# Optimization experiments

Measured on AMD Instinct MI355X. Metric: run time of the kernel, lower is better.

The kernel has to match this reference:

```python
import jax, jax.numpy as jnp
import numpy as np

# Constants from the torch module
S_DECAY = 0.95    # sentence_decay
P_DECAY = 0.99    # paragraph_decay
D_DECAY = 0.999   # document_decay
ALPHA = 0.1       # delta_update alpha for sentence/paragraph
DOC_ALPHA = 0.05  # delta_update alpha for document
BETA = 1.0
PARA_GROUP = 5    # sentences per paragraph
EPS = 1e-12       # F.normalize eps


def _normalize(x):
    # matches torch.nn.functional.normalize(x, dim=-1)
    return x / jnp.maximum(jnp.linalg.norm(x, axis=-1, keepdims=True), EPS)


def _delta_step(M, kn, v, alpha, beta):
    # M: [H, dk, dv]; kn: [dk] (already L2-normalized); v: [dv]
    # M_new = M @ (I - alpha * kn kn^T) + beta * kn v^T   (erase matrix is symmetric,
    # so the einsum 'hkv,hkj->hjv' form equals this rank-1 update -- no dk x dk matrix needed)
    kTM = jnp.einsum('k,hkv->hv', kn, M)                       # [H, dv]
    return M - alpha * kn[None, :, None] * kTM[:, None, :] \
             + beta * (kn[:, None] * v[None, :])[None, :, :]


def _scan_updates(M0, K, V, decay, alpha, beta):
    # Streaming delta-rule: per step, decay then erase/write.
    def step(M, kv):
        k, v = kv
        M = M * decay
        M = _delta_step(M, _normalize(k), v, alpha, beta)
        return M, None
    M, _ = jax.lax.scan(step, M0, (K, V))
    return M


def setup_inputs() -> dict:
    key = jax.random.key(0)
    ks = jax.random.split(key, 7)
    T, d_emb, d_k, d_v, H = 1000, 768, 256, 256, 8
    emb = jax.random.normal(ks[0], (T, d_emb), dtype=jnp.float32)
    q = jax.random.normal(ks[1], (d_k,), dtype=jnp.float32)
    W_k = jax.random.normal(ks[2], (d_emb, d_k), dtype=jnp.float32) * 0.02
    b_k = jax.random.normal(ks[3], (d_k,), dtype=jnp.float32) * 0.02
    W_v = jax.random.normal(ks[4], (d_emb, d_v), dtype=jnp.float32) * 0.02
    b_v = jax.random.normal(ks[5], (d_v,), dtype=jnp.float32) * 0.02
    M_sent0 = jnp.zeros((H, d_k, d_v), dtype=jnp.float32)
    M_para0 = jnp.zeros((H, d_k, d_v), dtype=jnp.float32)
    M_doc0 = jnp.zeros((H, d_k, d_v), dtype=jnp.float32)
    return {"emb": emb, "q": q, "W_k": W_k, "b_k": b_k, "W_v": W_v, "b_v": b_v,
            "M_sent0": M_sent0, "M_para0": M_para0, "M_doc0": M_doc0}


def reference(emb, q, W_k, b_k, W_v, b_v, M_sent0, M_para0, M_doc0):
    T, d_emb = emb.shape
    # Level 1: sentence memory -- one delta update per sentence embedding
    K = emb @ W_k + b_k            # [T, dk]
    V = emb @ W_v + b_v            # [T, dv]
    M_sent = _scan_updates(M_sent0, K, V, S_DECAY, ALPHA, BETA)
    # Level 2: paragraph memory -- mean of each group of 5 sentence embeddings
    para_emb = emb.reshape(T // PARA_GROUP, PARA_GROUP, d_emb).mean(axis=1)
    PK = para_emb @ W_k + b_k
    PV = para_emb @ W_v + b_v
    M_para = _scan_updates(M_para0, PK, PV, P_DECAY, ALPHA, BETA)
    # Level 3: document memory -- single update from paragraph-memory statistics
    doc_k = M_para.mean(axis=0).mean(axis=-1)   # [dk]
    doc_v = M_para.mean(axis=0).mean(axis=0)    # [dv]
    M_doc = M_doc0 * D_DECAY
    M_doc = _delta_step(M_doc, _normalize(doc_k), doc_v, DOC_ALPHA, BETA)
    # recall(q, level='all')
    qn = _normalize(q)
    def recall(M):
        return jnp.einsum('hkv,k->hv', M, qn).mean(axis=0)   # [dv]
    return 0.2 * recall(M_sent) + 0.3 * recall(M_para) + 0.5 * recall(M_doc)
```

## Files before the change

kernel.cpp:

```cpp
#include <hip/hip_runtime.h>
#include <hip/hip_bf16.h>

#define ALPHA   0.1f
#define S_DECAY 0.95f
#define P_DECAY 0.99f
#define D_EMB   768
#define DK      256

template<int ctrl, int row_mask>
__device__ __forceinline__ float dpp_add(float x) {
    int y = __builtin_amdgcn_update_dpp(0, __float_as_int(x), ctrl, row_mask, 0xF, true);
    return x + __int_as_float(y);
}

template<int N>
__device__ __forceinline__ void wave_allred_arr(float (&x)[N]) {
#pragma unroll
    for (int n = 0; n < N; ++n) x[n] = dpp_add<0xB1,  0xF>(x[n]);
#pragma unroll
    for (int n = 0; n < N; ++n) x[n] = dpp_add<0x4E,  0xF>(x[n]);
#pragma unroll
    for (int n = 0; n < N; ++n) x[n] = dpp_add<0x141, 0xF>(x[n]);
#pragma unroll
    for (int n = 0; n < N; ++n) x[n] = dpp_add<0x140, 0xF>(x[n]);
#pragma unroll
    for (int n = 0; n < N; ++n) x[n] = dpp_add<0x142, 0xA>(x[n]);
#pragma unroll
    for (int n = 0; n < N; ++n) x[n] = dpp_add<0x143, 0xC>(x[n]);
#pragma unroll
    for (int n = 0; n < N; ++n)
        x[n] = __int_as_float(__builtin_amdgcn_readlane(__float_as_int(x[n]), 63));
}

__device__ __forceinline__ float dot4v(const float4& a, const float4& b) {
    float t0 = a.x * b.x; t0 = fmaf(a.y, b.y, t0);
    float t1 = a.z * b.z; t1 = fmaf(a.w, b.w, t1);
    return t0 + t1;
}

__device__ __forceinline__ float rl(float x, int lane) {
    return __int_as_float(__builtin_amdgcn_readlane(__float_as_int(x), lane));
}

__global__ __launch_bounds__(256) void prep_kernel(
    const float* __restrict__ emb,
    const float* __restrict__ Wk, const float* __restrict__ bk,
    const float* __restrict__ Wv, const float* __restrict__ bv,
    float* __restrict__ K, float* __restrict__ V, float* __restrict__ USrev,
    float* __restrict__ out, int T)
{
    const int tid = threadIdx.x;
    const int bid = blockIdx.x;
    const int NBLK = (T / 4) * 2;
    if (bid >= NBLK) {
        const int PADS = ((T + 63) / 64) * 64;
        for (int i = tid; i < (PADS - T) * DK; i += 256) USrev[(size_t)T * DK + i] = 0.f;
        out[tid] = 0.f;
        return;
    }
    const int mat = bid & 1;
    const int r0  = (bid >> 1) * 4;

    __shared__ float se[4][D_EMB];
    __shared__ float s_red[4][4];

    const float4* emb4 = reinterpret_cast<const float4*>(emb);
#pragma unroll
    for (int r = 0; r < 4; ++r) {
        if (tid < D_EMB / 4)
            reinterpret_cast<float4*>(se[r])[tid] = emb4[(size_t)(r0 + r) * (D_EMB / 4) + tid];
    }
    __syncthreads();

    const float* Wp = mat ? Wv : Wk;
    const float* bp = mat ? bv : bk;
    const int j = tid;

    float a0 = 0.f, a1 = 0.f, a2 = 0.f, a3 = 0.f;
    float c0 = Wp[j],        c1 = Wp[j + DK],     c2 = Wp[j + 2*DK], c3 = Wp[j + 3*DK];
    float p0 = Wp[j + 4*DK], p1 = Wp[j + 5*DK],   p2 = Wp[j + 6*DK], p3 = Wp[j + 7*DK];

    for (int d = 0; d < D_EMB; d += 4) {
        int dn = d + 8; if (dn >= D_EMB) dn = 0;
        const float* wn = Wp + (size_t)dn * DK + j;
        float n0 = wn[0], n1 = wn[DK], n2 = wn[2*DK], n3 = wn[3*DK];

        float4 e0 = *reinterpret_cast<const float4*>(&se[0][d]);
        float4 e1 = *reinterpret_cast<const float4*>(&se[1][d]);
        float4 e2 = *reinterpret_cast<const float4*>(&se[2][d]);
        float4 e3 = *reinterpret_cast<const float4*>(&se[3][d]);

        a0 = fmaf(e0.x, c0, a0); a0 = fmaf(e0.y, c1, a0);
        a0 = fmaf(e0.z, c2, a0); a0 = fmaf(e0.w, c3, a0);
        a1 = fmaf(e1.x, c0, a1); a1 = fmaf(e1.y, c1, a1);
        a1 = fmaf(e1.z, c2, a1); a1 = fmaf(e1.w, c3, a1);
        a2 = fmaf(e2.x, c0, a2); a2 = fmaf(e2.y, c1, a2);
        a2 = fmaf(e2.z, c2, a2); a2 = fmaf(e2.w, c3, a2);
        a3 = fmaf(e3.x, c0, a3); a3 = fmaf(e3.y, c1, a3);
        a3 = fmaf(e3.z, c2, a3); a3 = fmaf(e3.w, c3, a3);

        c0 = p0; c1 = p1; c2 = p2; c3 = p3;
        p0 = n0; p1 = n1; p2 = n2; p3 = n3;
    }

    float bj = bp[j];
    float o0 = a0 + bj, o1 = a1 + bj, o2 = a2 + bj, o3 = a3 + bj;
    float* dst = mat ? V : K;
    dst[(size_t)(r0 + 0) * DK + j] = o0;
    dst[(size_t)(r0 + 1) * DK + j] = o1;
    dst[(size_t)(r0 + 2) * DK + j] = o2;
    dst[(size_t)(r0 + 3) * DK + j] = o3;

    if (mat == 0) {
        const int wave = tid >> 6, l = tid & 63;
        float red[4] = { o0*o0, o1*o1, o2*o2, o3*o3 };
        wave_allred_arr(red);
        if (l == 0) {
            s_red[wave][0] = red[0]; s_red[wave][1] = red[1];
            s_red[wave][2] = red[2]; s_red[wave][3] = red[3];
        }
        __syncthreads();
        float t0 = s_red[0][0] + s_red[1][0] + s_red[2][0] + s_red[3][0];
        float t1 = s_red[0][1] + s_red[1][1] + s_red[2][1] + s_red[3][1];
        float t2 = s_red[0][2] + s_red[1][2] + s_red[2][2] + s_red[3][2];
        float t3 = s_red[0][3] + s_red[1][3] + s_red[2][3] + s_red[3][3];
        USrev[(size_t)(T - 1 - (r0 + 0)) * DK + j] = o0 * (1.0f / fmaxf(sqrtf(t0), 1e-12f));
        USrev[(size_t)(T - 1 - (r0 + 1)) * DK + j] = o1 * (1.0f / fmaxf(sqrtf(t1), 1e-12f));
        USrev[(size_t)(T - 1 - (r0 + 2)) * DK + j] = o2 * (1.0f / fmaxf(sqrtf(t2), 1e-12f));
        USrev[(size_t)(T - 1 - (r0 + 3)) * DK + j] = o3 * (1.0f / fmaxf(sqrtf(t3), 1e-12f));
    }
}

#define SU_STRIDE 260
__global__ __launch_bounds__(256) void graminv_kernel(
    const float* __restrict__ K, const float* __restrict__ V,
    const float* __restrict__ USrev,
    float* __restrict__ UPrev, float* __restrict__ UPfwd,
    float* __restrict__ PV, float* __restrict__ SVv,
    float* __restrict__ AinvT, float* __restrict__ F1, float* __restrict__ biasF,
    int P, int NCS, int NCP)
{
    __shared__ float sU[64 * SU_STRIDE];
    __shared__ float sA[64 * 65];
    __shared__ float sX[64 * 65];
    __shared__ float s_sv[64];
    __shared__ float s_pd[64];
    __shared__ float4 s_f1w[4][64];
    const int tid = threadIdx.x, wv = tid >> 6, l = tid & 63;
    const int bid = blockIdx.x;
    int type, m;
    if (bid < NCS)            { type = 0; m = bid; }
    else if (bid < NCS + NCP) { type = 1; m = bid - NCS; }
    else                      { type = 2; m = bid - NCS - NCP; }

    if (tid < 64) s_pd[tid] = powf(P_DECAY, (float)tid);

    float4 f1p = make_float4(0.f, 0.f, 0.f, 0.f);

    if (type == 0) {
        const float4* U4 = reinterpret_cast<const float4*>(USrev) + (size_t)m * 4096;
        for (int idx = tid; idx < 4096; idx += 256) {
            float4 t = U4[idx];
            int row = idx >> 6, c4 = (idx & 63) << 2;
            *reinterpret_cast<float4*>(&sU[row * SU_STRIDE + c4]) = t;
        }
    } else if (type == 1) {
        const float4* K4 = reinterpret_cast<const float4*>(K);
        for (int ii = 0; ii < 16; ++ii) {
            int i = wv * 16 + ii;
            int p = P - 1 - (64 * m + i);
            float4 u = make_float4(0.f, 0.f, 0.f, 0.f);
            if (p >= 0) {
                float4 pk = make_float4(0.f, 0.f, 0.f, 0.f);
#pragma unroll
                for (int s = 0; s < 5; ++s) {
                    float4 k4 = K4[(size_t)(5 * p + s) * 64 + l];
                    pk.x += k4.x; pk.y += k4.y; pk.z += k4.z; pk.w += k4.w;
                }
                pk.x *= 0.2f; pk.y *= 0.2f; pk.z *= 0.2f; pk.w *= 0.2f;
                float red[1] = { dot4v(pk, pk) };
                wave_allred_arr(red);
                float inv = 1.0f / fmaxf(sqrtf(red[0]), 1e-12f);
                u = make_float4(pk.x * inv, pk.y * inv, pk.z * inv, pk.w * inv);
            }
            *reinterpret_cast<float4*>(&sU[i * SU_STRIDE + 4 * l]) = u;
            reinterpret_cast<float4*>(UPrev)[(size_t)(64 * m + i) * 64 + l] = u;
        }
    } else {
        const float4* K4 = reinterpret_cast<const float4*>(K);
        const float4* V4 = reinterpret_cast<const float4*>(V);
        for (int ii = 0; ii < 16; ++ii) {
            int i = wv * 16 + ii;
            int p = 64 * m + i;
            float4 u = make_float4(0.f, 0.f, 0.f, 0.f);
            float sv = 0.f;
            if (p < P) {
                float4 pk = make_float4(0.f, 0.f, 0.f, 0.f);
                float4 pv = make_float4(0.f, 0.f, 0.f, 0.f);
#pragma unroll
                for (int s = 0; s < 5; ++s) {
                    float4 k4 = K4[(size_t)(5 * p + s) * 64 + l];
                    float4 v4 = V4[(size_t)(5 * p + s) * 64 + l];
                    pk.x += k4.x; pk.y += k4.y; pk.z += k4.z; pk.w += k4.w;
                    pv.x += v4.x; pv.y += v4.y; pv.z += v4.z; pv.w += v4.w;
                }
                pk.x *= 0.2f; pk.y *= 0.2f; pk.z *= 0.2f; pk.w *= 0.2f;
                pv.x *= 0.2f; pv.y *= 0.2f; pv.z *= 0.2f; pv.w *= 0.2f;
                reinterpret_cast<float4*>(PV)[(size_t)p * 64 + l] = pv;
                float red[2] = { dot4v(pk, pk), pv.x + pv.y + pv.z + pv.w };
                wave_allred_arr(red);
                float inv = 1.0f / fmaxf(sqrtf(red[0]), 1e-12f);
                u = make_float4(pk.x * inv, pk.y * inv, pk.z * inv, pk.w * inv);
                sv = red[1];
            }
            *reinterpret_cast<float4*>(&sU[i * SU_STRIDE + 4 * l]) = u;
            reinterpret_cast<float4*>(UPfwd)[(size_t)(64 * m + i) * 64 + l] = u;
            if (l == 0) { s_sv[i] = sv; SVv[64 * m + i] = sv; }
            float f = powf(P_DECAY, (float)(63 - i)) * sv;
            f1p.x = fmaf(f, u.x, f1p.x); f1p.y = fmaf(f, u.y, f1p.y);
            f1p.z = fmaf(f, u.z, f1p.z); f1p.w = fmaf(f, u.w, f1p.w);
        }
        s_f1w[wv][l] = f1p;
    }
    __syncthreads();

    if (type == 2 && wv == 0) {
        float4 a = s_f1w[0][l], b = s_f1w[1][l], c = s_f1w[2][l], d = s_f1w[3][l];
        float4 tot = make_float4(a.x+b.x+c.x+d.x, a.y+b.y+c.y+d.y,
                                 a.z+b.z+c.z+d.z, a.w+b.w+c.w+d.w);
        reinterpret_cast<float4*>(F1)[(size_t)m * 64 + l] = tot;
    }

    const int tr = tid & 15, tcg = tid >> 4;
    const int i0 = tr * 4, j0 = tcg * 4;
    if (tcg <= tr) {
        float g[4][4];
#pragma unroll
        for (int r = 0; r < 4; ++r)
#pragma unroll
            for (int c = 0; c < 4; ++c) g[r][c] = 0.f;
        for (int k4 = 0; k4 < 64; ++k4) {
            float4 A0 = *reinterpret_cast<const float4*>(&sU[(i0    ) * SU_STRIDE + 4*k4]);
            float4 A1 = *reinterpret_cast<const float4*>(&sU[(i0 + 1) * SU_STRIDE + 4*k4]);
            float4 A2 = *reinterpret_cast<const float4*>(&sU[(i0 + 2) * SU_STRIDE + 4*k4]);
            float4 A3 = *reinterpret_cast<const float4*>(&sU[(i0 + 3) * SU_STRIDE + 4*k4]);
            float4 B0 = *reinterpret_cast<const float4*>(&sU[(j0    ) * SU_STRIDE + 4*k4]);
            float4 B1 = *reinterpret_cast<const float4*>(&sU[(j0 + 1) * SU_STRIDE + 4*k4]);
            float4 B2 = *reinterpret_cast<const float4*>(&sU[(j0 + 2) * SU_STRIDE + 4*k4]);
            float4 B3 = *reinterpret_cast<const float4*>(&sU[(j0 + 3) * SU_STRIDE + 4*k4]);
            g[0][0] += dot4v(A0, B0); g[0][1] += dot4v(A0, B1);
            g[0][2] += dot4v(A0, B2); g[0][3] += dot4v(A0, B3);
            g[1][0] += dot4v(A1, B0); g[1][1] += dot4v(A1, B1);
            g[1][2] += dot4v(A1, B2); g[1][3] += dot4v(A1, B3);
            g[2][0] += dot4v(A2, B0); g[2][1] += dot4v(A2, B1);
            g[2][2] += dot4v(A2, B2); g[2][3] += dot4v(A2, B3);
            g[3][0] += dot4v(A3, B0); g[3][1] += dot4v(A3, B1);
            g[3][2] += dot4v(A3, B2); g[3][3] += dot4v(A3, B3);
        }
#pragma unroll
        for (int r = 0; r < 4; ++r)
#pragma unroll
            for (int c = 0; c < 4; ++c) {
                int gi = i0 + r, gj = j0 + c;
                float val = 0.f;
                if (gj < gi) {
                    val = ALPHA * g[r][c];
                    if (type == 2) val *= s_pd[gi - gj];
                }
                sA[gi * 65 + gj] = val;
            }
    } else {
#pragma unroll
        for (int r = 0; r < 4; ++r)
#pragma unroll
            for (int c = 0; c < 4; ++c)
                sA[(i0 + r) * 65 + j0 + c] = 0.f;
    }
    __syncthreads();

    if (type == 2 && wv == 0) {
        float dotb = 0.f;
#pragma unroll
        for (int jj = 0; jj < 64; ++jj)
            dotb = fmaf(sA[l * 65 + jj], s_sv[jj], dotb);
        biasF[m * 64 + l] = dotb * (1.0f / ALPHA);
    }

    {
        const int base = wv * 16;
        float x[16];
#pragma unroll
        for (int r = 0; r < 16; ++r) x[r] = (base + r == l) ? 1.f : 0.f;
        for (int s = 0; s < 4; ++s) {
            if (wv == s) {
#pragma unroll
                for (int i = 1; i < 16; ++i)
#pragma unroll
                    for (int jj = 0; jj < 16; ++jj)
                        if (jj < i)
                            x[i] = fmaf(-sA[(base + i) * 65 + (base + jj)], x[jj], x[i]);
#pragma unroll
                for (int r = 0; r < 16; ++r) sX[(base + r) * 65 + l] = x[r];
            }
            __syncthreads();
            if (wv > s) {
#pragma unroll
                for (int i = 0; i < 16; ++i) {
                    float xi = sX[(s * 16 + i) * 65 + l];
#pragma unroll
                    for (int r = 0; r < 16; ++r)
                        x[r] = fmaf(-sA[(base + r) * 65 + (s * 16 + i)], xi, x[r]);
                }
            }
        }
    }
    __syncthreads();

    float* dstA = AinvT + (size_t)bid * 4096;
    for (int idx = tid; idx < 4096; idx += 256) {
        int jcol = idx >> 6, irow = idx & 63;
        dstA[idx] = sX[irow * 65 + jcol];
    }
}

__global__ __launch_bounds__(512) void solve_kernel(
    const float* __restrict__ USrev, const float* __restrict__ UPrev,
    const float* __restrict__ UPfwd, const float* __restrict__ AinvT,
    const float* __restrict__ F1, const float* __restrict__ biasF,
    const float* __restrict__ q,
    float* __restrict__ BS, float* __restrict__ BPB1, float* __restrict__ BPB2,
    float* __restrict__ gscal, int NCS, int NCP)
{
    __shared__ float s_cp[8][64], s_cp2[8][64];
    __shared__ float4 s_part[8][64], s_part2[8][64];
    __shared__ float s_powd[65];
    const int tid = threadIdx.x, wave = tid >> 6, l = tid & 63;
    const int wb = wave * 8;
    if (tid <= 64) s_powd[tid] = powf(P_DECAY, (float)tid);

    float4 q4 = reinterpret_cast<const float4*>(q)[l];
    float qs[1] = { dot4v(q4, q4) };
    wave_allred_arr(qs);
    float qinv = 1.0f / fmaxf(sqrtf(qs[0]), 1e-12f);
    float4 qn = make_float4(q4.x * qinv, q4.y * qinv, q4.z * qinv, q4.w * qinv);
    __syncthreads();

    if (blockIdx.x == 0) {
        float4 w1 = qn;
        const float4* U4 = reinterpret_cast<const float4*>(USrev);
        float4 curU[8]; float curX[8];
#pragma unroll
        for (int r = 0; r < 8; ++r) {
            curU[r] = U4[(size_t)(wb + r) * 64 + l];
            curX[r] = AinvT[(size_t)(wb + r) * 64 + l];
        }
        for (int m = 0; m < NCS; ++m) {
            float4 nxtU[8]; float nxtX[8];
            if (m + 1 < NCS) {
#pragma unroll
                for (int r = 0; r < 8; ++r) {
                    nxtU[r] = U4[(size_t)(m + 1) * 4096 + (size_t)(wb + r) * 64 + l];
                    nxtX[r] = AinvT[(size_t)(m + 1) * 4096 + (size_t)(wb + r) * 64 + l];
                }
            }
            float d[8];
#pragma unroll
            for (int r = 0; r < 8; ++r) d[r] = dot4v(curU[r], w1);
            wave_allred_arr(d);
            if (l == 0) {
#pragma unroll
                for (int r = 0; r < 8; ++r) BS[m * 64 + wb + r] = d[r];
            }
            float cp = 0.f;
#pragma unroll
            for (int r = 0; r < 8; ++r) cp = fmaf(curX[r], d[r], cp);
            s_cp[wave][l] = cp;
            __syncthreads();
            float cl = 0.f;
#pragma unroll
            for (int w = 0; w < 8; ++w) cl += s_cp[w][l];
            float4 part = make_float4(0.f, 0.f, 0.f, 0.f);
#pragma unroll
            for (int r = 0; r < 8; ++r) {
                float ci = rl(cl, wb + r);
                part.x = fmaf(ci, curU[r].x, part.x); part.y = fmaf(ci, curU[r].y, part.y);
                part.z = fmaf(ci, curU[r].z, part.z); part.w = fmaf(ci, curU[r].w, part.w);
            }
            s_part[wave][l] = part;
            __syncthreads();
            float4 s = make_float4(0.f, 0.f, 0.f, 0.f);
#pragma unroll
            for (int w = 0; w < 8; ++w) {
                float4 p = s_part[w][l];
                s.x += p.x; s.y += p.y; s.z += p.z; s.w += p.w;
            }
            w1.x = fmaf(-ALPHA, s.x, w1.x); w1.y = fmaf(-ALPHA, s.y, w1.y);
            w1.z = fmaf(-ALPHA, s.z, w1.z); w1.w = fmaf(-ALPHA, s.w, w1.w);
            if (m + 1 < NCS) {
#pragma unroll
                for (int r = 0; r < 8; ++r) { curU[r] = nxtU[r]; curX[r] = nxtX[r]; }
            }
        }
    } else {
        {
            float4 w1 = qn;
            float4 w2 = make_float4(1.f, 1.f, 1.f, 1.f);
            const float4* U4 = reinterpret_cast<const float4*>(UPrev);
            float4 curU[8]; float curX[8];
#pragma unroll
            for (int r = 0; r < 8; ++r) {
                curU[r] = U4[(size_t)(wb + r) * 64 + l];
                curX[r] = AinvT[(size_t)NCS * 4096 + (size_t)(wb + r) * 64 + l];
            }
            for (int m = 0; m < NCP; ++m) {
                float4 nxtU[8]; float nxtX[8];
                if (m + 1 < NCP) {
#pragma unroll
                    for (int r = 0; r < 8; ++r) {
                        nxtU[r] = U4[(size_t)(m + 1) * 4096 + (size_t)(wb + r) * 64 + l];
                        nxtX[r] = AinvT[(size_t)(NCS + m + 1) * 4096 + (size_t)(wb + r) * 64 + l];
                    }
                }
                float d[16];
#pragma unroll
                for (int r = 0; r < 8; ++r) {
                    d[r]     = dot4v(curU[r], w1);
                    d[8 + r] = dot4v(curU[r], w2);
                }
                wave_allred_arr(d);
                if (l == 0) {
#pragma unroll
                    for (int r = 0; r < 8; ++r) {
                        BPB1[m * 64 + wb + r] = d[r];
                        BPB2[m * 64 + wb + r] = d[8 + r];
                    }
                }
                float cp1 = 0.f, cp2 = 0.f;
#pragma unroll
                for (int r = 0; r < 8; ++r) {
                    cp1 = fmaf(curX[r], d[r], cp1);
                    cp2 = fmaf(curX[r], d[8 + r], cp2);
                }
                s_cp[wave][l] = cp1; s_cp2[wave][l] = cp2;
                __syncthreads();
                float cl1 = 0.f, cl2 = 0.f;
#pragma unroll
                for (int w = 0; w < 8; ++w) { cl1 += s_cp[w][l]; cl2 += s_cp2[w][l]; }
                float4 p1 = make_float4(0.f,0.f,0.f,0.f), p2 = make_float4(0.f,0.f,0.f,0.f);
#pragma unroll
                for (int r = 0; r < 8; ++r) {
                    float c1 = rl(cl1, wb + r), c2 = rl(cl2, wb + r);
                    p1.x = fmaf(c1, curU[r].x, p1.x); p1.y = fmaf(c1, curU[r].y, p1.y);
                    p1.z = fmaf(c1, curU[r].z, p1.z); p1.w = fmaf(c1, curU[r].w, p1.w);
                    p2.x = fmaf(c2, curU[r].x, p2.x); p2.y = fmaf(c2, curU[r].y, p2.y);
                    p2.z = fmaf(c2, curU[r].z, p2.z); p2.w = fmaf(c2, curU[r].w, p2.w);
                }
                s_part[wave][l] = p1; s_part2[wave][l] = p2;
                __syncthreads();
                float4 s1 = make_float4(0.f,0.f,0.f,0.f), s2 = make_float4(0.f,0.f,0.f,0.f);
#pragma unroll
                for (int w = 0; w < 8; ++w) {
                    float4 a = s_part[w][l];  float4 b = s_part2[w][l];
                    s1.x += a.x; s1.y += a.y; s1.z += a.z; s1.w += a.w;
                    s2.x += b.x; s2.y += b.y; s2.z += b.z; s2.w += b.w;
                }
                w1.x = fmaf(-ALPHA, s1.x, w1.x); w1.y = fmaf(-ALPHA, s1.y, w1.y);
                w1.z = fmaf(-ALPHA, s1.z, w1.z); w1.w = fmaf(-ALPHA, s1.w, w1.w);
                w2.x = fmaf(-ALPHA, s2.x, w2.x); w2.y = fmaf(-ALPHA, s2.y, w2.y);
                w2.z = fmaf(-ALPHA, s2.z, w2.z); w2.w = fmaf(-ALPHA, s2.w, w2.w);
                if (m + 1 < NCP) {
#pragma unroll
                    for (int r = 0; r < 8; ++r) { curU[r] = nxtU[r]; curX[r] = nxtX[r]; }
                }
            }
        }
        __syncthreads();
        float4 y = make_float4(0.f, 0.f, 0.f, 0.f);
        {
            const float4* U4 = reinterpret_cast<const float4*>(UPfwd);
            float4 curU[8]; float curX[8];
#pragma unroll
            for (int r = 0; r < 8; ++r) {
                curU[r] = U4[(size_t)(wb + r) * 64 + l];
                curX[r] = AinvT[(size_t)(NCS + NCP) * 4096 + (size_t)(wb + r) * 64 + l];
            }
            for (int m = 0; m < NCP; ++m) {
                float4 nxtU[8]; float nxtX[8];
                if (m + 1 < NCP) {
#pragma unroll
                    for (int r = 0; r < 8; ++r) {
                        nxtU[r] = U4[(size_t)(m + 1) * 4096 + (size_t)(wb + r) * 64 + l];
                        nxtX[r] = AinvT[(size_t)(NCS + NCP + m + 1) * 4096 + (size_t)(wb + r) * 64 + l];
                    }
                }
                float biasr[8];
#pragma unroll
                for (int r = 0; r < 8; ++r) biasr[r] = biasF[m * 64 + wb + r];
                float4 f1 = reinterpret_cast<const float4*>(F1)[(size_t)m * 64 + l];
                float d[8];
#pragma unroll
                for (int r = 0; r < 8; ++r) d[r] = dot4v(curU[r], y);
                wave_allred_arr(d);
#pragma unroll
                for (int r = 0; r < 8; ++r)
                    d[r] = fmaf(s_powd[wb + r + 1], d[r], biasr[r]);
                float cp = 0.f;
#pragma unroll
                for (int r = 0; r < 8; ++r) cp = fmaf(curX[r], d[r], cp);
                s_cp[wave][l] = cp;
                __syncthreads();
                float cl = 0.f;
#pragma unroll
                for (int w = 0; w < 8; ++w) cl += s_cp[w][l];
                float4 part = make_float4(0.f, 0.f, 0.f, 0.f);
#pragma unroll
                for (int r = 0; r < 8; ++r) {
                    float ci = s_powd[63 - (wb + r)] * rl(cl, wb + r);
                    part.x = fmaf(ci, curU[r].x, part.x); part.y = fmaf(ci, curU[r].y, part.y);
                    part.z = fmaf(ci, curU[r].z, part.z); part.w = fmaf(ci, curU[r].w, part.w);
                }
                s_part[wave][l] = part;
                __syncthreads();
                float4 s = make_float4(0.f, 0.f, 0.f, 0.f);
#pragma unroll
                for (int w = 0; w < 8; ++w) {
                    float4 p = s_part[w][l];
                    s.x += p.x; s.y += p.y; s.z += p.z; s.w += p.w;
                }
                float d64 = s_powd[64];
                y.x = fmaf(d64, y.x, fmaf(-ALPHA, s.x, f1.x));
                y.y = fmaf(d64, y.y, fmaf(-ALPHA, s.y, f1.y));
                y.z = fmaf(d64, y.z, fmaf(-ALPHA, s.z, f1.z));
                y.w = fmaf(d64, y.w, fmaf(-ALPHA, s.w, f1.w));
                if (m + 1 < NCP) {
#pragma unroll
                    for (int r = 0; r < 8; ++r) { curU[r] = nxtU[r]; curX[r] = nxtX[r]; }
                }
            }
        }
        float fin[2] = { dot4v(y, y), dot4v(qn, y) };
        wave_allred_arr(fin);
        if (tid == 0) gscal[0] = fin[1] / fmaxf(sqrtf(fin[0]), 2.56e-10f);
    }
}

__global__ __launch_bounds__(256) void accum_kernel(
    const float* __restrict__ V, const float* __restrict__ PV,
    const float* __restrict__ AinvT,
    const float* __restrict__ BS, const float* __restrict__ BPB1,
    const float* __restrict__ BPB2, const float* __restrict__ gscal,
    float* __restrict__ out, int T, int P, int NCS, int NCP)
{
    __shared__ float s_b[64], s_cp[4][64], wc[64];
    const int b = blockIdx.x, t = threadIdx.x;
    const float* src; const float* B; int i0, realN, chunk, ci; float decay;
    if (b < NCS)            { src = V;  B = BS;   ci = b;             realN = T; decay = S_DECAY; chunk = b; }
    else if (b < NCS + NCP) { src = PV; B = BPB1; ci = b - NCS;       realN = P; decay = P_DECAY; chunk = b; }
    else                    { src = PV; B = BPB2; ci = b - NCS - NCP; realN = P; decay = P_DECAY; chunk = b - NCP; }
    i0 = ci * 64;
    if (t < 64) s_b[t] = B[ci * 64 + t];
    __syncthreads();
    {
        const int part = t >> 6, k = t & 63;
        const float* Xc = AinvT + (size_t)chunk * 4096;
        float cp = 0.f;
#pragma unroll
        for (int jj = 0; jj < 16; ++jj) {
            int j = part * 16 + jj;
            cp = fmaf(Xc[j * 64 + k], s_b[j], cp);
        }
        s_cp[part][k] = cp;
    }
    __syncthreads();
    if (t < 64) {
        float c = s_cp[0][t] + s_cp[1][t] + s_cp[2][t] + s_cp[3][t];
        wc[t] = powf(decay, (float)(i0 + t)) * c;
    }
    __syncthreads();
    const int k = t;
    float acc = 0.f;
    for (int ii = 0; ii < 64; ++ii) {
        int i = i0 + ii;
        if (i < realN)
            acc = fmaf(wc[ii], src[(size_t)(realN - 1 - i) * DK + k], acc);
    }
    float wlev;
    if (b < NCS)            wlev = 0.2f;
    else if (b < NCS + NCP) wlev = 0.3f;
    else                    wlev = (0.5f / 256.0f) * gscal[0];
    atomicAdd(&out[k], wlev * acc);
}

extern "C" void kernel_launch(void* const* d_in, const int* in_sizes, int n_in,
                              void* d_out, int out_size, void* d_ws, size_t ws_size,
                              hipStream_t stream) {
    const float* emb = (const float*)d_in[0];
    const float* q   = (const float*)d_in[1];
    const float* Wk  = (const float*)d_in[2];
    const float* bk  = (const float*)d_in[3];
    const float* Wv  = (const float*)d_in[4];
    const float* bv  = (const float*)d_in[5];

    const int T = in_sizes[0] / D_EMB;
    const int P = T / 5;
    const int NCS  = (T + 63) / 64;
    const int NCP  = (P + 63) / 64;
    const int PADS = NCS * 64;
    const int PADP = NCP * 64;
    const int NCH  = NCS + 2 * NCP;

    float* ws    = (float*)d_ws;
    float* K     = ws;
    float* V     = K     + (size_t)T * DK;
    float* PV    = V     + (size_t)T * DK;
    float* USrev = PV    + (size_t)PADP * DK;
    float* UPrev = USrev + (size_t)PADS * DK;
    float* UPfwd = UPrev + (size_t)PADP * DK;
    float* SVv   = UPfwd + (size_t)PADP * DK;
    float* AinvT = SVv   + PADP;
    float* F1    = AinvT + (size_t)NCH * 4096;
    float* biasF = F1    + (size_t)NCP * 256;
    float* BS    = biasF + PADP;
    float* BPB1  = BS    + PADS;
    float* BPB2  = BPB1  + PADP;
    float* gscal = BPB2  + PADP;

    prep_kernel<<<(T / 4) * 2 + 1, 256, 0, stream>>>(emb, Wk, bk, Wv, bv,
                                                     K, V, USrev, (float*)d_out, T);
    graminv_kernel<<<NCH, 256, 0, stream>>>(K, V, USrev, UPrev, UPfwd,
                                            PV, SVv, AinvT, F1, biasF, P, NCS, NCP);
    solve_kernel<<<2, 512, 0, stream>>>(USrev, UPrev, UPfwd, AinvT, F1, biasF, q,
                                        BS, BPB1, BPB2, gscal, NCS, NCP);
    accum_kernel<<<NCH, 256, 0, stream>>>(V, PV, AinvT, BS, BPB1, BPB2, gscal,
                                          (float*)d_out, T, P, NCS, NCP);
}
```

Measured before the change: 188.4 us.

## Split fused gram-inverse kernel into fill, gram, and inverse kernels

The single graminv kernel, which built U rows, computed the chunk Gram matrix and inverted the triangular system in one block per chunk, becomes three kernels. A fill kernel builds the paragraph U rows, a gram kernel spreads each chunk's Gram product over four blocks (16-row slabs) reading B rows from global memory, and an inverse kernel does the triangular solve. The goal is more parallelism and less LDS per block for the Gram phase. In exchange it adds two kernel launches and a round trip of the Gram matrix and U through global memory.

```diff
diff --git a/kernel.cpp b/kernel.cpp
--- a/kernel.cpp
+++ b/kernel.cpp
@@ -131,41 +131,25 @@
     }
 }
 
-#define SU_STRIDE 260
-__global__ __launch_bounds__(256) void graminv_kernel(
+__global__ __launch_bounds__(256) void ufill_kernel(
     const float* __restrict__ K, const float* __restrict__ V,
-    const float* __restrict__ USrev,
     float* __restrict__ UPrev, float* __restrict__ UPfwd,
-    float* __restrict__ PV, float* __restrict__ SVv,
-    float* __restrict__ AinvT, float* __restrict__ F1, float* __restrict__ biasF,
-    int P, int NCS, int NCP)
+    float* __restrict__ PV, float* __restrict__ SVv, float* __restrict__ F1,
+    int P, int NCP)
 {
-    __shared__ float sU[64 * SU_STRIDE];
-    __shared__ float sA[64 * 65];
-    __shared__ float sX[64 * 65];
-    __shared__ float s_sv[64];
     __shared__ float s_pd[64];
     __shared__ float4 s_f1w[4][64];
     const int tid = threadIdx.x, wv = tid >> 6, l = tid & 63;
     const int bid = blockIdx.x;
-    int type, m;
-    if (bid < NCS)            { type = 0; m = bid; }
-    else if (bid < NCS + NCP) { type = 1; m = bid - NCS; }
-    else                      { type = 2; m = bid - NCS - NCP; }
+    const int type = (bid < NCP) ? 1 : 2;
+    const int m = (type == 1) ? bid : bid - NCP;
 
     if (tid < 64) s_pd[tid] = powf(P_DECAY, (float)tid);
-
-    float4 f1p = make_float4(0.f, 0.f, 0.f, 0.f);
-
-    if (type == 0) {
-        const float4* U4 = reinterpret_cast<const float4*>(USrev) + (size_t)m * 4096;
-        for (int idx = tid; idx < 4096; idx += 256) {
-            float4 t = U4[idx];
-            int row = idx >> 6, c4 = (idx & 63) << 2;
-            *reinterpret_cast<float4*>(&sU[row * SU_STRIDE + c4]) = t;
-        }
-    } else if (type == 1) {
-        const float4* K4 = reinterpret_cast<const float4*>(K);
+    __syncthreads();
+
+    const float4* K4 = reinterpret_cast<const float4*>(K);
+
+    if (type == 1) {
         for (int ii = 0; ii < 16; ++ii) {
             int i = wv * 16 + ii;
             int p = P - 1 - (64 * m + i);
@@ -183,12 +167,11 @@
                 float inv = 1.0f / fmaxf(sqrtf(red[0]), 1e-12f);
                 u = make_float4(pk.x * inv, pk.y * inv, pk.z * inv, pk.w * inv);
             }
-            *reinterpret_cast<float4*>(&sU[i * SU_STRIDE + 4 * l]) = u;
             reinterpret_cast<float4*>(UPrev)[(size_t)(64 * m + i) * 64 + l] = u;
         }
     } else {
-        const float4* K4 = reinterpret_cast<const float4*>(K);
         const float4* V4 = reinterpret_cast<const float4*>(V);
+        float4 f1p = make_float4(0.f, 0.f, 0.f, 0.f);
         for (int ii = 0; ii < 16; ++ii) {
             int i = wv * 16 + ii;
             int p = 64 * m + i;
@@ -213,69 +196,95 @@
                 u = make_float4(pk.x * inv, pk.y * inv, pk.z * inv, pk.w * inv);
                 sv = red[1];
             }
-            *reinterpret_cast<float4*>(&sU[i * SU_STRIDE + 4 * l]) = u;
             reinterpret_cast<float4*>(UPfwd)[(size_t)(64 * m + i) * 64 + l] = u;
-            if (l == 0) { s_sv[i] = sv; SVv[64 * m + i] = sv; }
-            float f = powf(P_DECAY, (float)(63 - i)) * sv;
+            if (l == 0) SVv[64 * m + i] = sv;
+            float f = s_pd[63 - i] * sv;
             f1p.x = fmaf(f, u.x, f1p.x); f1p.y = fmaf(f, u.y, f1p.y);
             f1p.z = fmaf(f, u.z, f1p.z); f1p.w = fmaf(f, u.w, f1p.w);
         }
         s_f1w[wv][l] = f1p;
-    }
-    __syncthreads();
-
-    if (type == 2 && wv == 0) {
-        float4 a = s_f1w[0][l], b = s_f1w[1][l], c = s_f1w[2][l], d = s_f1w[3][l];
-        float4 tot = make_float4(a.x+b.x+c.x+d.x, a.y+b.y+c.y+d.y,
-                                 a.z+b.z+c.z+d.z, a.w+b.w+c.w+d.w);
-        reinterpret_cast<float4*>(F1)[(size_t)m * 64 + l] = tot;
-    }
-
-    const int tr = tid & 15, tcg = tid >> 4;
-    const int i0 = tr * 4, j0 = tcg * 4;
-    if (tcg <= tr) {
-        float g[4][4];
-#pragma unroll
-        for (int r = 0; r < 4; ++r)
-#pragma unroll
-            for (int c = 0; c < 4; ++c) g[r][c] = 0.f;
-        for (int k4 = 0; k4 < 64; ++k4) {
-            float4 A0 = *reinterpret_cast<const float4*>(&sU[(i0    ) * SU_STRIDE + 4*k4]);
-            float4 A1 = *reinterpret_cast<const float4*>(&sU[(i0 + 1) * SU_STRIDE + 4*k4]);
-            float4 A2 = *reinterpret_cast<const float4*>(&sU[(i0 + 2) * SU_STRIDE + 4*k4]);
-            float4 A3 = *reinterpret_cast<const float4*>(&sU[(i0 + 3) * SU_STRIDE + 4*k4]);
-            float4 B0 = *reinterpret_cast<const float4*>(&sU[(j0    ) * SU_STRIDE + 4*k4]);
-            float4 B1 = *reinterpret_cast<const float4*>(&sU[(j0 + 1) * SU_STRIDE + 4*k4]);
-            float4 B2 = *reinterpret_cast<const float4*>(&sU[(j0 + 2) * SU_STRIDE + 4*k4]);
-            float4 B3 = *reinterpret_cast<const float4*>(&sU[(j0 + 3) * SU_STRIDE + 4*k4]);
-            g[0][0] += dot4v(A0, B0); g[0][1] += dot4v(A0, B1);
-            g[0][2] += dot4v(A0, B2); g[0][3] += dot4v(A0, B3);
-            g[1][0] += dot4v(A1, B0); g[1][1] += dot4v(A1, B1);
-            g[1][2] += dot4v(A1, B2); g[1][3] += dot4v(A1, B3);
-            g[2][0] += dot4v(A2, B0); g[2][1] += dot4v(A2, B1);
-            g[2][2] += dot4v(A2, B2); g[2][3] += dot4v(A2, B3);
-            g[3][0] += dot4v(A3, B0); g[3][1] += dot4v(A3, B1);
-            g[3][2] += dot4v(A3, B2); g[3][3] += dot4v(A3, B3);
-        }
-#pragma unroll
-        for (int r = 0; r < 4; ++r)
-#pragma unroll
-            for (int c = 0; c < 4; ++c) {
-                int gi = i0 + r, gj = j0 + c;
-                float val = 0.f;
-                if (gj < gi) {
-                    val = ALPHA * g[r][c];
-                    if (type == 2) val *= s_pd[gi - gj];
-                }
-                sA[gi * 65 + gj] = val;
-            }
-    } else {
-#pragma unroll
-        for (int r = 0; r < 4; ++r)
-#pragma unroll
-            for (int c = 0; c < 4; ++c)
-                sA[(i0 + r) * 65 + j0 + c] = 0.f;
-    }
+        __syncthreads();
+        if (wv == 0) {
+            float4 a = s_f1w[0][l], b = s_f1w[1][l], c = s_f1w[2][l], d = s_f1w[3][l];
+            float4 tot = make_float4(a.x+b.x+c.x+d.x, a.y+b.y+c.y+d.y,
+                                     a.z+b.z+c.z+d.z, a.w+b.w+c.w+d.w);
+            reinterpret_cast<float4*>(F1)[(size_t)m * 64 + l] = tot;
+        }
+    }
+}
+
+#define GS_STRIDE 260
+__global__ __launch_bounds__(256) void gram_kernel(
+    const float* __restrict__ USrev, const float* __restrict__ UPrev,
+    const float* __restrict__ UPfwd, float* __restrict__ Agram,
+    int NCS, int NCP)
+{
+    __shared__ float sAr[16 * GS_STRIDE];
+    __shared__ float s_pd[64];
+    const int tid = threadIdx.x;
+    const int chunk = blockIdx.x >> 2;
+    const int slab  = blockIdx.x & 3;
+    int type, m;
+    if (chunk < NCS)            { type = 0; m = chunk; }
+    else if (chunk < NCS + NCP) { type = 1; m = chunk - NCS; }
+    else                        { type = 2; m = chunk - NCS - NCP; }
+    const float* Ug = (type == 0) ? USrev + (size_t)m * 64 * DK
+                    : (type == 1) ? UPrev + (size_t)m * 64 * DK
+                                  : UPfwd + (size_t)m * 64 * DK;
+    const float4* Ug4 = reinterpret_cast<const float4*>(Ug);
+
+    for (int idx = tid; idx < 16 * 64; idx += 256) {
+        int r = idx >> 6, c4 = idx & 63;
+        float4 t = Ug4[(size_t)(slab * 16 + r) * 64 + c4];
+        *reinterpret_cast<float4*>(&sAr[r * GS_STRIDE + 4 * c4]) = t;
+    }
+    if (tid < 64) s_pd[tid] = powf(P_DECAY, (float)tid);
+    __syncthreads();
+
+    const int ti = tid & 15;
+    const int tj = tid >> 4;
+    const int gi = slab * 16 + ti;
+    const int j0 = tj * 4;
+
+    const float4* B0 = Ug4 + (size_t)(j0 + 0) * 64;
+    const float4* B1 = Ug4 + (size_t)(j0 + 1) * 64;
+    const float4* B2 = Ug4 + (size_t)(j0 + 2) * 64;
+    const float4* B3 = Ug4 + (size_t)(j0 + 3) * 64;
+
+    float g0 = 0.f, g1 = 0.f, g2 = 0.f, g3 = 0.f;
+    for (int k4 = 0; k4 < 64; ++k4) {
+        float4 a  = *reinterpret_cast<const float4*>(&sAr[ti * GS_STRIDE + 4 * k4]);
+        float4 b0 = B0[k4], b1 = B1[k4], b2 = B2[k4], b3 = B3[k4];
+        g0 += dot4v(a, b0); g1 += dot4v(a, b1);
+        g2 += dot4v(a, b2); g3 += dot4v(a, b3);
+    }
+
+    float4 outv;
+    outv.x = (j0 + 0 < gi) ? (ALPHA * g0 * ((type == 2) ? s_pd[gi - (j0 + 0)] : 1.f)) : 0.f;
+    outv.y = (j0 + 1 < gi) ? (ALPHA * g1 * ((type == 2) ? s_pd[gi - (j0 + 1)] : 1.f)) : 0.f;
+    outv.z = (j0 + 2 < gi) ? (ALPHA * g2 * ((type == 2) ? s_pd[gi - (j0 + 2)] : 1.f)) : 0.f;
+    outv.w = (j0 + 3 < gi) ? (ALPHA * g3 * ((type == 2) ? s_pd[gi - (j0 + 3)] : 1.f)) : 0.f;
+    reinterpret_cast<float4*>(Agram + (size_t)chunk * 4096)[gi * 16 + tj] = outv;
+}
+
+__global__ __launch_bounds__(256) void inv_kernel(
+    float* __restrict__ AinvT, const float* __restrict__ SVv,
+    float* __restrict__ biasF, int NCS, int NCP)
+{
+    __shared__ float sA[64 * 65];
+    __shared__ float sX[64 * 65];
+    __shared__ float s_sv[64];
+    const int tid = threadIdx.x, wv = tid >> 6, l = tid & 63;
+    const int bid = blockIdx.x;
+    int type, m;
+    if (bid < NCS)            { type = 0; m = bid; }
+    else if (bid < NCS + NCP) { type = 1; m = bid - NCS; }
+    else                      { type = 2; m = bid - NCS - NCP; }
+
+    float* Ag = AinvT + (size_t)bid * 4096;
+    for (int idx = tid; idx < 4096; idx += 256)
+        sA[(idx >> 6) * 65 + (idx & 63)] = Ag[idx];
+    if (type == 2 && tid < 64) s_sv[tid] = SVv[m * 64 + tid];
     __syncthreads();
 
     if (type == 2 && wv == 0) {
@@ -316,10 +325,9 @@
     }
     __syncthreads();
 
-    float* dstA = AinvT + (size_t)bid * 4096;
     for (int idx = tid; idx < 4096; idx += 256) {
         int jcol = idx >> 6, irow = idx & 63;
-        dstA[idx] = sX[irow * 65 + jcol];
+        Ag[idx] = sX[irow * 65 + jcol];
     }
 }
 
@@ -627,8 +635,9 @@
 
     prep_kernel<<<(T / 4) * 2 + 1, 256, 0, stream>>>(emb, Wk, bk, Wv, bv,
                                                      K, V, USrev, (float*)d_out, T);
-    graminv_kernel<<<NCH, 256, 0, stream>>>(K, V, USrev, UPrev, UPfwd,
-                                            PV, SVv, AinvT, F1, biasF, P, NCS, NCP);
+    ufill_kernel<<<2 * NCP, 256, 0, stream>>>(K, V, UPrev, UPfwd, PV, SVv, F1, P, NCP);
+    gram_kernel<<<NCH * 4, 256, 0, stream>>>(USrev, UPrev, UPfwd, AinvT, NCS, NCP);
+    inv_kernel<<<NCH, 256, 0, stream>>>(AinvT, SVv, biasF, NCS, NCP);
     solve_kernel<<<2, 512, 0, stream>>>(USrev, UPrev, UPfwd, AinvT, F1, biasF, q,
                                         BS, BPB1, BPB2, gscal, NCS, NCP);
     accum_kernel<<<NCH, 256, 0, stream>>>(V, PV, AinvT, BS, BPB1, BPB2, gscal,
```

New measurement: 202.0 us. 1.07x slower.
